# Kernel tuning notes

Measured on AMD Instinct MI355X. Metric: run time of the kernel, lower is better.

The kernel has to match this reference:

```python
import jax, jax.numpy as jnp
import numpy as np


def setup_inputs() -> dict:
    key = jax.random.key(0)
    k1, k2 = jax.random.split(key)
    B, L, K, C = 8, 4096, 32, 64
    x = jax.random.normal(k1, (B, L, K, C), dtype=jnp.float32)
    mask = jax.random.randint(k2, (B, L, K, C), 0, 2, dtype=jnp.int32)
    return {"x": x, "mask": mask}


def reference(x, mask):
    # Masked mean over the sequence dim (axis=1), broadcast back to [B, L, K, C].
    # Equivalent to torch.mean(x[b, mask[b,:,k,c].bool(), k, c]) per (b,k,c),
    # with empty-mask NaNs replaced by 0.
    m = mask.astype(x.dtype)
    s = jnp.sum(x * m, axis=1)          # [B, K, C]
    cnt = jnp.sum(m, axis=1)            # [B, K, C]
    mean = jnp.where(cnt > 0, s / jnp.maximum(cnt, 1), jnp.zeros_like(s))
    return jnp.broadcast_to(mean[:, None, :, :], x.shape)
```

## Files before the change

kernel.cpp:

```cpp
#include <hip/hip_runtime.h>

#define B_DIM 8
#define L_DIM 4096
#define KC 2048
#define LCB  16
#define PT   512

typedef float f4 __attribute__((ext_vector_type(4)));
typedef int   i4 __attribute__((ext_vector_type(4)));

__global__ __launch_bounds__(PT) void partial_k(const float* __restrict__ x,
                                                const int* __restrict__ mask,
                                                float* __restrict__ psum,
                                                float* __restrict__ pcnt,
                                                int nseg, int lrows) {
    const int b   = blockIdx.x / nseg;
    const int seg = blockIdx.x % nseg;
    const int t   = threadIdx.x;

    const long base = ((long)b * L_DIM + (long)seg * lrows) * KC + t * 4;

    f4 s = {0.f, 0.f, 0.f, 0.f};
    f4 c = {0.f, 0.f, 0.f, 0.f};

    #pragma unroll 4
    for (int l = 0; l < lrows; ++l) {
        const f4 xv = __builtin_nontemporal_load(
                          (const f4*)(x + base + (long)l * KC));
        const i4 mv = *(const i4*)(mask + base + (long)l * KC);
        float m0 = (float)mv.x, m1 = (float)mv.y, m2 = (float)mv.z, m3 = (float)mv.w;
        s.x = fmaf(xv.x, m0, s.x);  c.x += m0;
        s.y = fmaf(xv.y, m1, s.y);  c.y += m1;
        s.z = fmaf(xv.z, m2, s.z);  c.z += m2;
        s.w = fmaf(xv.w, m3, s.w);  c.w += m3;
    }

    const long po = ((long)b * nseg + seg) * KC + t * 4;
    *(f4*)(&psum[po]) = s;
    *(f4*)(&pcnt[po]) = c;
}

__global__ __launch_bounds__(256) void mean_k(const float* __restrict__ psum,
                                              const float* __restrict__ pcnt,
                                              float* __restrict__ mean,
                                              int nseg) {
    const int i = blockIdx.x * 256 + threadIdx.x;
    const int b = i / KC;
    const int j = i % KC;

    float s = 0.f, c = 0.f;
    #pragma unroll 4
    for (int seg = 0; seg < nseg; ++seg) {
        const long o = ((long)b * nseg + seg) * KC + j;
        s += psum[o];
        c += pcnt[o];
    }
    mean[i] = (c > 0.f) ? (s / c) : 0.f;
}

__global__ __launch_bounds__(PT) void bcast_k(const float* __restrict__ mean,
                                              float* __restrict__ out) {
    const int blocks_per_b = L_DIM / LCB;
    const int b    = blockIdx.x / blocks_per_b;
    const int lseg = blockIdx.x % blocks_per_b;
    const int t    = threadIdx.x;

    const f4 v = *(const f4*)(&mean[(long)b * KC + t * 4]);

    const long base = ((long)b * L_DIM + (long)lseg * LCB) * KC + t * 4;
    #pragma unroll
    for (int l = 0; l < LCB; ++l)
        *(f4*)(out + base + (long)l * KC) = v;
}

extern "C" void kernel_launch(void* const* d_in, const int* in_sizes, int n_in,
                              void* d_out, int out_size, void* d_ws, size_t ws_size,
                              hipStream_t stream) {
    const float* x    = (const float*)d_in[0];
    const int*   mask = (const int*)d_in[1];
    float*       out  = (float*)d_out;
    float*       ws   = (float*)d_ws;

    int nseg = 128;
    while (nseg > 8 &&
           (size_t)(2ul * B_DIM * nseg * KC + B_DIM * KC) * 4ul > ws_size)
        nseg >>= 1;
    const int lrows = L_DIM / nseg;

    float* psum = ws;
    float* pcnt = ws + (long)B_DIM * nseg * KC;
    float* mean = ws + 2l * B_DIM * nseg * KC;

    partial_k<<<B_DIM * nseg, PT, 0, stream>>>(x, mask, psum, pcnt,
                                               nseg, lrows);

    mean_k<<<(B_DIM * KC) / 256, 256, 0, stream>>>(psum, pcnt, mean, nseg);

    bcast_k<<<B_DIM * (L_DIM / LCB), PT, 0, stream>>>(mean, out);
}
```

Measured before the change: 189.2 us.

## Overlap tail-batch reduction with broadcast writes in a mixed kernel

Splits the batches into two groups: batches 0-5 are reduced first, then one mixed kernel reduces batches 6-7 while other blocks broadcast the means for batches 0-5. A final mean and broadcast pass handles batches 6-7. The aim is to run the read-heavy reduction alongside the write-heavy broadcast and so use HBM read and write bandwidth together. In exchange it adds two more kernel launches and drops the fallback that shrank the segment count when the workspace was small, so it now assumes the workspace is large enough.

```diff
diff --git a/kernel.cpp b/kernel.cpp
--- a/kernel.cpp
+++ b/kernel.cpp
@@ -3,28 +3,27 @@
 #define B_DIM 8
 #define L_DIM 4096
 #define KC 2048
-#define LCB  16
 #define PT   512
+#define NSEG 128
+#define LROWS (L_DIM / NSEG)
+#define WBPB 128
+#define WROWS (L_DIM / WBPB)
 
 typedef float f4 __attribute__((ext_vector_type(4)));
 typedef int   i4 __attribute__((ext_vector_type(4)));
 
-__global__ __launch_bounds__(PT) void partial_k(const float* __restrict__ x,
-                                                const int* __restrict__ mask,
-                                                float* __restrict__ psum,
-                                                float* __restrict__ pcnt,
-                                                int nseg, int lrows) {
-    const int b   = blockIdx.x / nseg;
-    const int seg = blockIdx.x % nseg;
-    const int t   = threadIdx.x;
-
-    const long base = ((long)b * L_DIM + (long)seg * lrows) * KC + t * 4;
+__device__ __forceinline__ void reduce_duty(const float* __restrict__ x,
+                                            const int* __restrict__ mask,
+                                            float* __restrict__ psum,
+                                            float* __restrict__ pcnt,
+                                            int b, int seg, int t) {
+    const long base = ((long)b * L_DIM + (long)seg * LROWS) * KC + t * 4;
 
     f4 s = {0.f, 0.f, 0.f, 0.f};
     f4 c = {0.f, 0.f, 0.f, 0.f};
 
     #pragma unroll 4
-    for (int l = 0; l < lrows; ++l) {
+    for (int l = 0; l < LROWS; ++l) {
         const f4 xv = __builtin_nontemporal_load(
                           (const f4*)(x + base + (long)l * KC));
         const i4 mv = *(const i4*)(mask + base + (long)l * KC);
@@ -35,42 +34,67 @@
         s.w = fmaf(xv.w, m3, s.w);  c.w += m3;
     }
 
-    const long po = ((long)b * nseg + seg) * KC + t * 4;
+    const long po = ((long)b * NSEG + seg) * KC + t * 4;
     *(f4*)(&psum[po]) = s;
     *(f4*)(&pcnt[po]) = c;
+}
+
+__device__ __forceinline__ void bcast_duty(const float* __restrict__ mean,
+                                           float* __restrict__ out,
+                                           int b, int seg, int t) {
+    const f4 v = *(const f4*)(&mean[(long)b * KC + t * 4]);
+    const long base = ((long)b * L_DIM + (long)seg * WROWS) * KC + t * 4;
+    #pragma unroll
+    for (int l = 0; l < WROWS; ++l)
+        *(f4*)(out + base + (long)l * KC) = v;
+}
+
+__global__ __launch_bounds__(PT) void partialA_k(const float* __restrict__ x,
+                                                 const int* __restrict__ mask,
+                                                 float* __restrict__ psum,
+                                                 float* __restrict__ pcnt) {
+    reduce_duty(x, mask, psum, pcnt, blockIdx.x / NSEG, blockIdx.x % NSEG,
+                threadIdx.x);
 }
 
 __global__ __launch_bounds__(256) void mean_k(const float* __restrict__ psum,
                                               const float* __restrict__ pcnt,
                                               float* __restrict__ mean,
-                                              int nseg) {
+                                              int b0) {
     const int i = blockIdx.x * 256 + threadIdx.x;
-    const int b = i / KC;
+    const int b = b0 + i / KC;
     const int j = i % KC;
 
     float s = 0.f, c = 0.f;
     #pragma unroll 4
-    for (int seg = 0; seg < nseg; ++seg) {
-        const long o = ((long)b * nseg + seg) * KC + j;
+    for (int seg = 0; seg < NSEG; ++seg) {
+        const long o = ((long)b * NSEG + seg) * KC + j;
         s += psum[o];
         c += pcnt[o];
     }
-    mean[i] = (c > 0.f) ? (s / c) : 0.f;
+    mean[(long)b * KC + j] = (c > 0.f) ? (s / c) : 0.f;
 }
 
-__global__ __launch_bounds__(PT) void bcast_k(const float* __restrict__ mean,
-                                              float* __restrict__ out) {
-    const int blocks_per_b = L_DIM / LCB;
-    const int b    = blockIdx.x / blocks_per_b;
-    const int lseg = blockIdx.x % blocks_per_b;
-    const int t    = threadIdx.x;
+__global__ __launch_bounds__(PT) void mix_k(const float* __restrict__ x,
+                                            const int* __restrict__ mask,
+                                            float* __restrict__ psum,
+                                            float* __restrict__ pcnt,
+                                            const float* __restrict__ mean,
+                                            float* __restrict__ out) {
+    const int t = threadIdx.x;
+    if (blockIdx.x < 2 * NSEG) {
+        const int bi = blockIdx.x;
+        reduce_duty(x, mask, psum, pcnt, 6 + bi / NSEG, bi % NSEG, t);
+    } else {
+        const int wb = blockIdx.x - 2 * NSEG;
+        bcast_duty(mean, out, wb / WBPB, wb % WBPB, t);
+    }
+}
 
-    const f4 v = *(const f4*)(&mean[(long)b * KC + t * 4]);
-
-    const long base = ((long)b * L_DIM + (long)lseg * LCB) * KC + t * 4;
-    #pragma unroll
-    for (int l = 0; l < LCB; ++l)
-        *(f4*)(out + base + (long)l * KC) = v;
+__global__ __launch_bounds__(PT) void bcastB_k(const float* __restrict__ mean,
+                                               float* __restrict__ out) {
+    bcast_duty(mean, out, 6 + blockIdx.x / WBPB, blockIdx.x % WBPB,
+               threadIdx.x);
 }
 
 extern "C" void kernel_launch(void* const* d_in, const int* in_sizes, int n_in,
@@ -81,20 +105,18 @@
     float*       out  = (float*)d_out;
     float*       ws   = (float*)d_ws;
 
-    int nseg = 128;
-    while (nseg > 8 &&
-           (size_t)(2ul * B_DIM * nseg * KC + B_DIM * KC) * 4ul > ws_size)
-        nseg >>= 1;
-    const int lrows = L_DIM / nseg;
+    float* psum = ws;
+    float* pcnt = ws + (long)B_DIM * NSEG * KC;
+    float* mean = ws + 2l * B_DIM * NSEG * KC;
 
-    float* psum = ws;
-    float* pcnt = ws + (long)B_DIM * nseg * KC;
-    float* mean = ws + 2l * B_DIM * nseg * KC;
+    partialA_k<<<6 * NSEG, PT, 0, stream>>>(x, mask, psum, pcnt);
 
-    partial_k<<<B_DIM * nseg, PT, 0, stream>>>(x, mask, psum, pcnt,
-                                               nseg, lrows);
+    mean_k<<<6 * KC / 256, 256, 0, stream>>>(psum, pcnt, mean, 0);
 
-    mean_k<<<(B_DIM * KC) / 256, 256, 0, stream>>>(psum, pcnt, mean, nseg);
+    mix_k<<<2 * NSEG + 6 * WBPB, PT, 0, stream>>>(x, mask, psum, pcnt,
+                                                  mean, out);
 
-    bcast_k<<<B_DIM * (L_DIM / LCB), PT, 0, stream>>>(mean, out);
+    mean_k<<<2 * KC / 256, 256, 0, stream>>>(psum, pcnt, mean, 6);
+
+    bcastB_k<<<2 * WBPB, PT, 0, stream>>>(mean, out);
 }
```

Measured after the change: 198.7 us. 5.0% more time.
